# Kernel tuning notes

Measured on AMD Instinct MI355X. Metric: run time of the kernel, lower is better.

Reference implementation:

```python
import jax, jax.numpy as jnp
import numpy as np

B, S, D_IN, D_OUT = 2, 2048, 4096, 4096


def setup_inputs() -> dict:
    key = jax.random.key(0)
    kx, kw, kb = jax.random.split(key, 3)
    x = jax.random.normal(kx, (B, S, D_IN), dtype=jnp.float32)
    weight = jax.random.normal(kw, (D_OUT, D_IN), dtype=jnp.float32)
    bias = jax.random.normal(kb, (D_OUT,), dtype=jnp.float32)
    return {"x": x, "weight": weight, "bias": bias}


def reference(x, weight, bias):
    # FdaBinary forward is simply sign(); linear with binarized weight.
    w_bin = jnp.sign(weight)  # [D_OUT, D_IN], values in {-1, 0, +1}
    # F.linear: x @ w.T + b
    out = jnp.einsum("bsd,od->bso", x, w_bin) + bias
    return out
```

## Files before the change

### kernel.cpp

```cpp
#include <hip/hip_runtime.h>
#include <hip/hip_bf16.h>
#include <stdint.h>
#include <stddef.h>

#define M_DIM 4096
#define N_DIM 4096
#define K_DIM 4096
#define BM 128
#define BN 128
#define BK 64
#define NKT (K_DIM / BK)

typedef __bf16 bf16;
typedef __attribute__((ext_vector_type(4))) __bf16 bf16x4;
typedef __attribute__((ext_vector_type(8))) __bf16 bf16x8;
typedef __attribute__((ext_vector_type(4))) float f32x4;

__global__ __launch_bounds__(256) void prep_kernel(const float* __restrict__ x,
                                                   const float* __restrict__ w,
                                                   bf16* __restrict__ xb,
                                                   bf16* __restrict__ wb) {
    const int idx = blockIdx.x * 256 + threadIdx.x;
    float4 xv = ((const float4*)x)[idx];
    bf16x4 xo;
    xo[0] = (bf16)xv.x; xo[1] = (bf16)xv.y; xo[2] = (bf16)xv.z; xo[3] = (bf16)xv.w;
    ((bf16x4*)xb)[idx] = xo;

    float4 wv = ((const float4*)w)[idx];
    bf16x4 wo;
    wo[0] = (bf16)((wv.x > 0.f) ? 1.f : ((wv.x < 0.f) ? -1.f : 0.f));
    wo[1] = (bf16)((wv.y > 0.f) ? 1.f : ((wv.y < 0.f) ? -1.f : 0.f));
    wo[2] = (bf16)((wv.z > 0.f) ? 1.f : ((wv.z < 0.f) ? -1.f : 0.f));
    wo[3] = (bf16)((wv.w > 0.f) ? 1.f : ((wv.w < 0.f) ? -1.f : 0.f));
    ((bf16x4*)wb)[idx] = wo;
}

__device__ __forceinline__ void load_lds16(const void* g, void* l) {
    __builtin_amdgcn_global_load_lds(
        (const __attribute__((address_space(1))) void*)g,
        (__attribute__((address_space(3))) void*)l, 16, 0, 0);
}

__global__ __launch_bounds__(256) void gemm_bin_kernel(const bf16* __restrict__ A,
                                                       const bf16* __restrict__ Bw,
                                                       const float* __restrict__ bias,
                                                       float* __restrict__ C) {
    __shared__ __align__(16) bf16 As[BM * BK];
    __shared__ __align__(16) bf16 Bs[BN * BK];

    const int tid  = threadIdx.x;
    const int lane = tid & 63;
    const int wave = tid >> 6;
    const int wm   = wave & 1;
    const int wn   = wave >> 1;

    const int tileM = blockIdx.y * BM;
    const int tileN = blockIdx.x * BN;

    const int rowInC = lane >> 3;
    const int q_src  = (lane & 7) ^ rowInC;

    const bf16* gA[4];
    const bf16* gB[4];
    bf16* lA[4];
    bf16* lB[4];
#pragma unroll
    for (int t = 0; t < 4; ++t) {
        const int c = wave * 4 + t;
        gA[t] = A  + (size_t)(tileM + c * 8 + rowInC) * K_DIM + q_src * 8;
        gB[t] = Bw + (size_t)(tileN + c * 8 + rowInC) * K_DIM + q_src * 8;
        lA[t] = As + c * 512;
        lB[t] = Bs + c * 512;
    }

    f32x4 acc[4][4];
#pragma unroll
    for (int i = 0; i < 4; ++i)
#pragma unroll
        for (int j = 0; j < 4; ++j)
            acc[i][j] = (f32x4){0.f, 0.f, 0.f, 0.f};

    const int l15 = lane & 15;
    const int qf  = lane >> 4;
    const int fragRowA = wm * 64 + l15;
    const int fragRowB = wn * 64 + l15;

    for (int kt = 0; kt < NKT; ++kt) {
#pragma unroll
        for (int t = 0; t < 4; ++t) {
            load_lds16(gA[t], lA[t]);
            load_lds16(gB[t], lB[t]);
            gA[t] += BK; gB[t] += BK;
        }

        __syncthreads();

#pragma unroll
        for (int kk = 0; kk < 2; ++kk) {
            const int s = (kk * 4 + qf) ^ (l15 & 7);
            bf16x8 af[4], bfr[4];
#pragma unroll
            for (int i = 0; i < 4; ++i)
                af[i] = *(const bf16x8*)&As[(fragRowA + i * 16) * BK + s * 8];
#pragma unroll
            for (int j = 0; j < 4; ++j)
                bfr[j] = *(const bf16x8*)&Bs[(fragRowB + j * 16) * BK + s * 8];

#pragma unroll
            for (int i = 0; i < 4; ++i)
#pragma unroll
                for (int j = 0; j < 4; ++j)
                    acc[i][j] = __builtin_amdgcn_mfma_f32_16x16x32_bf16(af[i], bfr[j], acc[i][j], 0, 0, 0);
        }

        __syncthreads();
    }

#pragma unroll
    for (int j = 0; j < 4; ++j) {
        const int col = tileN + wn * 64 + j * 16 + l15;
        const float bv = bias[col];
#pragma unroll
        for (int i = 0; i < 4; ++i) {
            const int row0 = tileM + wm * 64 + i * 16 + (qf << 2);
#pragma unroll
            for (int rr = 0; rr < 4; ++rr) {
                C[(size_t)(row0 + rr) * N_DIM + col] = acc[i][j][rr] + bv;
            }
        }
    }
}

extern "C" void kernel_launch(void* const* d_in, const int* in_sizes, int n_in,
                              void* d_out, int out_size, void* d_ws, size_t ws_size,
                              hipStream_t stream) {
    const float* x    = (const float*)d_in[0];
    const float* w    = (const float*)d_in[1];
    const float* bias = (const float*)d_in[2];
    float* out        = (float*)d_out;

    const int nElem = M_DIM * K_DIM;
    bf16* xb = (bf16*)d_ws;
    bf16* wb = xb + (size_t)nElem;

    prep_kernel<<<nElem / 4 / 256, 256, 0, stream>>>(x, w, xb, wb);

    dim3 grid(N_DIM / BN, M_DIM / BM);
    gemm_bin_kernel<<<grid, 256, 0, stream>>>(xb, wb, bias, out);
}
```

Measured before the change: 296.6 us.

## Fuse fp32-to-bf16 and sign conversion into GEMM with register-prefetched tiles

Removes the separate prep kernel that converted x to bf16 and binarized the weights through a workspace buffer. The GEMM now loads fp32 tiles of X and W directly, converts them in registers (sign via bit manipulation), and writes them into swizzled LDS. The next K tile is prefetched into registers while MFMAs run on the current one. The block grows to 512 threads, each wave computing a 64x32 sub-tile. The trade-off is twice the global/L2 bytes per tile and conversion work repeated across every tile that reuses the same data. Also, sign_pack maps exact zeros to +1 rather than 0.

```diff
diff --git a/kernel.cpp b/kernel.cpp
--- a/kernel.cpp
+++ b/kernel.cpp
@@ -10,41 +10,27 @@
 #define BN 128
 #define BK 64
 #define NKT (K_DIM / BK)
+#define K4  (K_DIM / 4)
 
 typedef __bf16 bf16;
-typedef __attribute__((ext_vector_type(4))) __bf16 bf16x4;
 typedef __attribute__((ext_vector_type(8))) __bf16 bf16x8;
 typedef __attribute__((ext_vector_type(4))) float f32x4;
 
-__global__ __launch_bounds__(256) void prep_kernel(const float* __restrict__ x,
-                                                   const float* __restrict__ w,
-                                                   bf16* __restrict__ xb,
-                                                   bf16* __restrict__ wb) {
-    const int idx = blockIdx.x * 256 + threadIdx.x;
-    float4 xv = ((const float4*)x)[idx];
-    bf16x4 xo;
-    xo[0] = (bf16)xv.x; xo[1] = (bf16)xv.y; xo[2] = (bf16)xv.z; xo[3] = (bf16)xv.w;
-    ((bf16x4*)xb)[idx] = xo;
-
-    float4 wv = ((const float4*)w)[idx];
-    bf16x4 wo;
-    wo[0] = (bf16)((wv.x > 0.f) ? 1.f : ((wv.x < 0.f) ? -1.f : 0.f));
-    wo[1] = (bf16)((wv.y > 0.f) ? 1.f : ((wv.y < 0.f) ? -1.f : 0.f));
-    wo[2] = (bf16)((wv.z > 0.f) ? 1.f : ((wv.z < 0.f) ? -1.f : 0.f));
-    wo[3] = (bf16)((wv.w > 0.f) ? 1.f : ((wv.w < 0.f) ? -1.f : 0.f));
-    ((bf16x4*)wb)[idx] = wo;
+__device__ __forceinline__ uint32_t pack_bf16(float a, float b) {
+    uint16_t ua = __builtin_bit_cast(uint16_t, (bf16)a);
+    uint16_t ub = __builtin_bit_cast(uint16_t, (bf16)b);
+    return (uint32_t)ua | ((uint32_t)ub << 16);
+}
+__device__ __forceinline__ uint32_t sign_pack(float a, float b) {
+    uint32_t ua = __builtin_bit_cast(uint32_t, a);
+    uint32_t ub = __builtin_bit_cast(uint32_t, b);
+    return 0x3F803F80u | ((ua >> 16) & 0x8000u) | (ub & 0x80000000u);
 }
 
-__device__ __forceinline__ void load_lds16(const void* g, void* l) {
-    __builtin_amdgcn_global_load_lds(
-        (const __attribute__((address_space(1))) void*)g,
-        (__attribute__((address_space(3))) void*)l, 16, 0, 0);
-}
-
-__global__ __launch_bounds__(256) void gemm_bin_kernel(const bf16* __restrict__ A,
-                                                       const bf16* __restrict__ Bw,
-                                                       const float* __restrict__ bias,
-                                                       float* __restrict__ C) {
+__global__ __launch_bounds__(512) void gemm_fused_kernel(
+    const float* __restrict__ X, const float* __restrict__ W,
+    const float* __restrict__ bias, float* __restrict__ C)
+{
     __shared__ __align__(16) bf16 As[BM * BK];
     __shared__ __align__(16) bf16 Bs[BN * BK];
 
@@ -57,68 +43,85 @@
     const int tileM = blockIdx.y * BM;
     const int tileN = blockIdx.x * BN;
 
-    const int rowInC = lane >> 3;
-    const int q_src  = (lane & 7) ^ rowInC;
+    const int rT = tid >> 4;
+    const int c4 = tid & 15;
+    const int sw = (c4 >> 1) ^ (rT & 7);
+    const uint32_t ldsOff = (uint32_t)rT * 128 + (uint32_t)sw * 16 + (uint32_t)(c4 & 1) * 8;
+    char* ldsA = (char*)As + ldsOff;
+    char* ldsB = (char*)Bs + ldsOff;
 
-    const bf16* gA[4];
-    const bf16* gB[4];
-    bf16* lA[4];
-    bf16* lB[4];
+    int offX[4], offW[4];
 #pragma unroll
-    for (int t = 0; t < 4; ++t) {
-        const int c = wave * 4 + t;
-        gA[t] = A  + (size_t)(tileM + c * 8 + rowInC) * K_DIM + q_src * 8;
-        gB[t] = Bw + (size_t)(tileN + c * 8 + rowInC) * K_DIM + q_src * 8;
-        lA[t] = As + c * 512;
-        lB[t] = Bs + c * 512;
+    for (int p = 0; p < 4; ++p) {
+        offX[p] = (tileM + p * 32 + rT) * K4 + c4;
+        offW[p] = (tileN + p * 32 + rT) * K4 + c4;
     }
+    const float4* X4 = (const float4*)X;
+    const float4* W4 = (const float4*)W;
 
-    f32x4 acc[4][4];
+    f32x4 acc[4][2];
 #pragma unroll
     for (int i = 0; i < 4; ++i)
 #pragma unroll
-        for (int j = 0; j < 4; ++j)
+        for (int j = 0; j < 2; ++j)
             acc[i][j] = (f32x4){0.f, 0.f, 0.f, 0.f};
 
     const int l15 = lane & 15;
     const int qf  = lane >> 4;
     const int fragRowA = wm * 64 + l15;
-    const int fragRowB = wn * 64 + l15;
+    const int fragRowB = wn * 32 + l15;
+
+    float4 ldA[4], ldB[4];
+#pragma unroll
+    for (int p = 0; p < 4; ++p) { ldA[p] = X4[offX[p]]; ldB[p] = W4[offW[p]]; }
 
     for (int kt = 0; kt < NKT; ++kt) {
+        uint2 stA[4], stB[4];
 #pragma unroll
-        for (int t = 0; t < 4; ++t) {
-            load_lds16(gA[t], lA[t]);
-            load_lds16(gB[t], lB[t]);
-            gA[t] += BK; gB[t] += BK;
+        for (int p = 0; p < 4; ++p) {
+            stA[p].x = pack_bf16(ldA[p].x, ldA[p].y);
+            stA[p].y = pack_bf16(ldA[p].z, ldA[p].w);
+            stB[p].x = sign_pack(ldB[p].x, ldB[p].y);
+            stB[p].y = sign_pack(ldB[p].z, ldB[p].w);
         }
+#pragma unroll
+        for (int p = 0; p < 4; ++p) {
+            *(uint2*)(ldsA + p * 4096) = stA[p];
+            *(uint2*)(ldsB + p * 4096) = stB[p];
+        }
+        __syncthreads();
 
-        __syncthreads();
+        if (kt + 1 < NKT) {
+            const int ko = (kt + 1) * 16;
+#pragma unroll
+            for (int p = 0; p < 4; ++p) {
+                ldA[p] = X4[offX[p] + ko];
+                ldB[p] = W4[offW[p] + ko];
+            }
+        }
 
 #pragma unroll
         for (int kk = 0; kk < 2; ++kk) {
             const int s = (kk * 4 + qf) ^ (l15 & 7);
-            bf16x8 af[4], bfr[4];
+            bf16x8 af[4], bfr[2];
 #pragma unroll
             for (int i = 0; i < 4; ++i)
                 af[i] = *(const bf16x8*)&As[(fragRowA + i * 16) * BK + s * 8];
 #pragma unroll
-            for (int j = 0; j < 4; ++j)
+            for (int j = 0; j < 2; ++j)
                 bfr[j] = *(const bf16x8*)&Bs[(fragRowB + j * 16) * BK + s * 8];
-
 #pragma unroll
             for (int i = 0; i < 4; ++i)
 #pragma unroll
-                for (int j = 0; j < 4; ++j)
+                for (int j = 0; j < 2; ++j)
                     acc[i][j] = __builtin_amdgcn_mfma_f32_16x16x32_bf16(af[i], bfr[j], acc[i][j], 0, 0, 0);
         }
-
         __syncthreads();
     }
 
 #pragma unroll
-    for (int j = 0; j < 4; ++j) {
-        const int col = tileN + wn * 64 + j * 16 + l15;
+    for (int j = 0; j < 2; ++j) {
+        const int col = tileN + wn * 32 + j * 16 + l15;
         const float bv = bias[col];
 #pragma unroll
         for (int i = 0; i < 4; ++i) {
@@ -139,12 +142,6 @@
     const float* bias = (const float*)d_in[2];
     float* out        = (float*)d_out;
 
-    const int nElem = M_DIM * K_DIM;
-    bf16* xb = (bf16*)d_ws;
-    bf16* wb = xb + (size_t)nElem;
-
-    prep_kernel<<<nElem / 4 / 256, 256, 0, stream>>>(x, w, xb, wb);
-
     dim3 grid(N_DIM / BN, M_DIM / BM);
-    gemm_bin_kernel<<<grid, 256, 0, stream>>>(xb, wb, bias, out);
+    gemm_fused_kernel<<<grid, 512, 0, stream>>>(x, w, bias, out);
 }
```

New measurement: 367.1 us. +23.8%, slower.
